# Kernel tuning notes

Measured on AMD Instinct MI355X. Metric: run time of the kernel, lower is better.

## Reference

```python
import jax, jax.numpy as jnp
import numpy as np

FEATURE_DIM = 256
NUM_COEDGES = 200000


def setup_inputs() -> dict:
    key = jax.random.key(0)
    ks = jax.random.split(key, 13)
    d = FEATURE_DIM
    n = NUM_COEDGES
    scale = 1.0 / np.sqrt(d)
    inp = {
        "features": jax.random.normal(ks[0], (n, d), dtype=jnp.float32),
        "next_indices": jax.random.randint(ks[1], (n,), 0, n),
        "prev_indices": jax.random.randint(ks[2], (n,), 0, n),
        "mate_indices": jax.random.randint(ks[3], (n,), 0, n),
        # Linear params (torch Linear: y = x @ W.T + b); store as [d, d] for x @ W
        "W_self": jax.random.uniform(ks[4], (d, d), jnp.float32, -scale, scale),
        "b_self": jax.random.uniform(ks[5], (d,), jnp.float32, -scale, scale),
        "W_next": jax.random.uniform(ks[6], (d, d), jnp.float32, -scale, scale),
        "b_next": jax.random.uniform(ks[7], (d,), jnp.float32, -scale, scale),
        "W_prev": jax.random.uniform(ks[8], (d, d), jnp.float32, -scale, scale),
        "b_prev": jax.random.uniform(ks[9], (d,), jnp.float32, -scale, scale),
        "W_mate": jax.random.uniform(ks[10], (d, d), jnp.float32, -scale, scale),
        "b_mate": jax.random.uniform(ks[11], (d,), jnp.float32, -scale, scale),
    }
    return inp


def reference(features, next_indices, prev_indices, mate_indices,
              W_self, b_self, W_next, b_next, W_prev, b_prev, W_mate, b_mate):
    h = features  # [n, d]
    h_self = h @ W_self + b_self
    h_next = h[next_indices] @ W_next + b_next
    h_prev = h[prev_indices] @ W_prev + b_prev
    h_mate = h[mate_indices] @ W_mate + b_mate
    return jax.nn.relu(h_self + h_next + h_prev + h_mate)
```

## Files before the change

### kernel.cpp

```cpp
#include <hip/hip_runtime.h>
#include <stdint.h>


#define D 256
#define BM 64

typedef __bf16 bf16x8 __attribute__((ext_vector_type(8)));
typedef float f32x4 __attribute__((ext_vector_type(4)));

static __device__ __forceinline__ uint16_t f32_to_bf16_rne(uint32_t u) {
    return (uint16_t)((u + 0x7FFFu + ((u >> 16) & 1u)) >> 16);
}

__global__ void k_conv(const float* __restrict__ f, uint16_t* __restrict__ o, long total) {
    long i = ((long)blockIdx.x * blockDim.x + threadIdx.x) * 8;
    if (i + 8 > total) return;
    const uint32_t* p = (const uint32_t*)(f + i);
    uint32_t v[8];
    *(uint4*)(v)     = *(const uint4*)(p);
    *(uint4*)(v + 4) = *(const uint4*)(p + 4);
    union { uint16_t u16[8]; uint4 v4; } r;
#pragma unroll
    for (int j = 0; j < 8; j++) r.u16[j] = f32_to_bf16_rne(v[j]);
    *(uint4*)(o + i) = r.v4;
}

__global__ void k_pack(const float* __restrict__ Ws, const float* __restrict__ Wn,
                       const float* __restrict__ Wp, const float* __restrict__ Wm,
                       uint16_t* __restrict__ Bp) {
    int b = blockIdx.x;
    int l = threadIdx.x;
    int ksg = b >> 4, nt = b & 15;
    int ph = ksg >> 3;
    const float* W = (ph == 0) ? Ws : (ph == 1) ? Wn : (ph == 2) ? Wp : Wm;
    int kl = (ksg & 7) * 32 + (l >> 4) * 8;
    int n  = nt * 16 + (l & 15);
    uint16_t* dst = Bp + ((size_t)b * 64 + l) * 8;
#pragma unroll
    for (int j = 0; j < 8; j++) {
        uint32_t u = __builtin_bit_cast(uint32_t, W[(size_t)(kl + j) * D + n]);
        dst[j] = f32_to_bf16_rne(u);
    }
}

__global__ void k_bias(const float* __restrict__ b0, const float* __restrict__ b1,
                       const float* __restrict__ b2, const float* __restrict__ b3,
                       float* __restrict__ btot) {
    int t = threadIdx.x;
    if (t < D) btot[t] = b0[t] + b1[t] + b2[t] + b3[t];
}

typedef __attribute__((address_space(1))) uint32_t gu32;
typedef __attribute__((address_space(3))) uint32_t lu32;

__global__ __launch_bounds__(256) void k_gemm(
    const uint16_t* __restrict__ fb,
    const int* __restrict__ ni, const int* __restrict__ pi, const int* __restrict__ mi,
    const uint16_t* __restrict__ Bp, const float* __restrict__ btot,
    float* __restrict__ out, int nrows)
{
    __shared__ uint16_t As[BM * D];
    const int t  = threadIdx.x;
    const int w  = t >> 6;
    const int l  = t & 63;
    const int ml = l & 15;
    const int q  = l >> 4;
    const int m0 = blockIdx.x * BM;

    f32x4 acc[4][4] = {};

    const int rpar = w * 16 + (l >> 5);
    const int cs   = l & 31;

    for (int p = 0; p < 4; p++) {
        const int* idx = (p == 0) ? (const int*)0 : (p == 1) ? ni : (p == 2) ? pi : mi;
        __syncthreads();
#pragma unroll
        for (int e = 0; e < 8; e++) {
            int r    = rpar + e * 2;
            int rowg = m0 + r;
            if (rowg >= nrows) rowg = nrows - 1;
            int gr = idx ? idx[rowg] : rowg;
            int cc = cs ^ (r & 7);
            const uint16_t* g = fb + (size_t)gr * D + cc * 8;
            uint16_t* s = &As[(w * 16 + e * 2) * D];
            __builtin_amdgcn_global_load_lds((gu32*)g, (lu32*)s, 16, 0, 0);
        }
        __syncthreads();

        const uint16_t* bbase = Bp + (((size_t)p * 128 + w * 4) * 64 + l) * 8;
#pragma unroll 2
        for (int ks = 0; ks < 8; ks++) {
            bf16x8 bfr[4];
#pragma unroll
            for (int j = 0; j < 4; j++)
                bfr[j] = *(const bf16x8*)(bbase + ((size_t)ks * 16 + j) * 64 * 8);
            bf16x8 afr[4];
#pragma unroll
            for (int mt = 0; mt < 4; mt++) {
                int r  = mt * 16 + ml;
                int ch = (ks * 4 + q) ^ (r & 7);
                afr[mt] = *(const bf16x8*)&As[r * D + ch * 8];
            }
#pragma unroll
            for (int mt = 0; mt < 4; mt++)
#pragma unroll
                for (int j = 0; j < 4; j++)
                    acc[mt][j] = __builtin_amdgcn_mfma_f32_16x16x32_bf16(
                        afr[mt], bfr[j], acc[mt][j], 0, 0, 0);
        }
    }

#pragma unroll
    for (int j = 0; j < 4; j++) {
        int n = (w * 4 + j) * 16 + ml;
        float bv = btot[n];
#pragma unroll
        for (int mt = 0; mt < 4; mt++) {
#pragma unroll
            for (int rg = 0; rg < 4; rg++) {
                int row = m0 + mt * 16 + q * 4 + rg;
                if (row < nrows) {
                    float v = acc[mt][j][rg] + bv;
                    out[(size_t)row * D + n] = v > 0.f ? v : 0.f;
                }
            }
        }
    }
}

__global__ void k_naive(const float* __restrict__ f,
                        const int* __restrict__ ni, const int* __restrict__ pi,
                        const int* __restrict__ mi,
                        const float* __restrict__ Ws, const float* __restrict__ bs,
                        const float* __restrict__ Wn, const float* __restrict__ bn,
                        const float* __restrict__ Wp, const float* __restrict__ bp,
                        const float* __restrict__ Wm, const float* __restrict__ bm,
                        float* __restrict__ out) {
    int row = blockIdx.x, n = threadIdx.x;
    const float* f0 = f + (size_t)row * D;
    const float* f1 = f + (size_t)ni[row] * D;
    const float* f2 = f + (size_t)pi[row] * D;
    const float* f3 = f + (size_t)mi[row] * D;
    float s = bs[n] + bn[n] + bp[n] + bm[n];
    for (int k = 0; k < D; k++)
        s += f0[k] * Ws[k * D + n] + f1[k] * Wn[k * D + n] +
             f2[k] * Wp[k * D + n] + f3[k] * Wm[k * D + n];
    out[(size_t)row * D + n] = s > 0.f ? s : 0.f;
}

extern "C" void kernel_launch(void* const* d_in, const int* in_sizes, int n_in,
                              void* d_out, int out_size, void* d_ws, size_t ws_size,
                              hipStream_t stream) {
    const float* feat = (const float*)d_in[0];
    const int*   ni   = (const int*)d_in[1];
    const int*   pi   = (const int*)d_in[2];
    const int*   mi   = (const int*)d_in[3];
    const float* Ws   = (const float*)d_in[4];
    const float* bs   = (const float*)d_in[5];
    const float* Wn   = (const float*)d_in[6];
    const float* bn   = (const float*)d_in[7];
    const float* Wp   = (const float*)d_in[8];
    const float* bp   = (const float*)d_in[9];
    const float* Wm   = (const float*)d_in[10];
    const float* bm   = (const float*)d_in[11];
    float* out = (float*)d_out;

    int nrows = in_sizes[1];
    size_t feat_elems = (size_t)nrows * D;
    size_t fb_bytes   = feat_elems * 2;
    size_t bp_off     = fb_bytes;
    size_t bias_off   = bp_off + (size_t)1024 * D * 2;
    size_t need       = bias_off + (size_t)D * 4;

    if (ws_size < need) {
        k_naive<<<nrows, D, 0, stream>>>(feat, ni, pi, mi, Ws, bs, Wn, bn, Wp, bp, Wm, bm, out);
        return;
    }

    uint16_t* fbuf = (uint16_t*)d_ws;
    uint16_t* Bpk  = (uint16_t*)((char*)d_ws + bp_off);
    float*    btot = (float*)((char*)d_ws + bias_off);

    long total = (long)feat_elems;
    int cblocks = (int)((total / 8 + 255) / 256);
    k_conv<<<cblocks, 256, 0, stream>>>(feat, fbuf, total);
    k_pack<<<512, 64, 0, stream>>>(Ws, Wn, Wp, Wm, Bpk);
    k_bias<<<1, 256, 0, stream>>>(bs, bn, bp, bm, btot);
    k_gemm<<<(nrows + BM - 1) / BM, 256, 0, stream>>>(fbuf, ni, pi, mi, Bpk, btot, out, nrows);
}
```

Baseline: 568.6 us.

## Double-buffer gathered A tiles in LDS and fuse prep kernels into one

```diff
diff --git a/kernel.cpp b/kernel.cpp
--- a/kernel.cpp
+++ b/kernel.cpp
@@ -12,54 +12,76 @@
     return (uint16_t)((u + 0x7FFFu + ((u >> 16) & 1u)) >> 16);
 }
 
-__global__ void k_conv(const float* __restrict__ f, uint16_t* __restrict__ o, long total) {
-    long i = ((long)blockIdx.x * blockDim.x + threadIdx.x) * 8;
-    if (i + 8 > total) return;
-    const uint32_t* p = (const uint32_t*)(f + i);
-    uint32_t v[8];
-    *(uint4*)(v)     = *(const uint4*)(p);
-    *(uint4*)(v + 4) = *(const uint4*)(p + 4);
-    union { uint16_t u16[8]; uint4 v4; } r;
-#pragma unroll
-    for (int j = 0; j < 8; j++) r.u16[j] = f32_to_bf16_rne(v[j]);
-    *(uint4*)(o + i) = r.v4;
-}
-
-__global__ void k_pack(const float* __restrict__ Ws, const float* __restrict__ Wn,
+__global__ void k_prep(const float* __restrict__ f, uint16_t* __restrict__ o, long total,
+                       const float* __restrict__ Ws, const float* __restrict__ Wn,
                        const float* __restrict__ Wp, const float* __restrict__ Wm,
-                       uint16_t* __restrict__ Bp) {
-    int b = blockIdx.x;
-    int l = threadIdx.x;
-    int ksg = b >> 4, nt = b & 15;
-    int ph = ksg >> 3;
-    const float* W = (ph == 0) ? Ws : (ph == 1) ? Wn : (ph == 2) ? Wp : Wm;
-    int kl = (ksg & 7) * 32 + (l >> 4) * 8;
-    int n  = nt * 16 + (l & 15);
-    uint16_t* dst = Bp + ((size_t)b * 64 + l) * 8;
-#pragma unroll
-    for (int j = 0; j < 8; j++) {
-        uint32_t u = __builtin_bit_cast(uint32_t, W[(size_t)(kl + j) * D + n]);
-        dst[j] = f32_to_bf16_rne(u);
-    }
-}
-
-__global__ void k_bias(const float* __restrict__ b0, const float* __restrict__ b1,
+                       uint16_t* __restrict__ Bp,
+                       const float* __restrict__ b0, const float* __restrict__ b1,
                        const float* __restrict__ b2, const float* __restrict__ b3,
                        float* __restrict__ btot) {
-    int t = threadIdx.x;
-    if (t < D) btot[t] = b0[t] + b1[t] + b2[t] + b3[t];
+    long i = ((long)blockIdx.x * blockDim.x + threadIdx.x) * 8;
+    if (i + 8 <= total) {
+        const uint32_t* p = (const uint32_t*)(f + i);
+        uint32_t v[8];
+        *(uint4*)(v)     = *(const uint4*)(p);
+        *(uint4*)(v + 4) = *(const uint4*)(p + 4);
+        union { uint16_t u16[8]; uint4 v4; } r;
+#pragma unroll
+        for (int j = 0; j < 8; j++) r.u16[j] = f32_to_bf16_rne(v[j]);
+        *(uint4*)(o + i) = r.v4;
+    }
+    if (blockIdx.x < 128) {
+        int b = blockIdx.x * 4 + (threadIdx.x >> 6);
+        int l = threadIdx.x & 63;
+        int ksg = b >> 4, nt = b & 15;
+        int ph = ksg >> 3;
+        const float* W = (ph == 0) ? Ws : (ph == 1) ? Wn : (ph == 2) ? Wp : Wm;
+        int kl = (ksg & 7) * 32 + (l >> 4) * 8;
+        int n  = nt * 16 + (l & 15);
+        uint16_t* dst = Bp + ((size_t)b * 64 + l) * 8;
+#pragma unroll
+        for (int j = 0; j < 8; j++) {
+            uint32_t u = __builtin_bit_cast(uint32_t, W[(size_t)(kl + j) * D + n]);
+            dst[j] = f32_to_bf16_rne(u);
+        }
+    } else if (blockIdx.x == 128) {
+        int t = threadIdx.x;
+        if (t < D) btot[t] = b0[t] + b1[t] + b2[t] + b3[t];
+    }
 }
 
 typedef __attribute__((address_space(1))) uint32_t gu32;
 typedef __attribute__((address_space(3))) uint32_t lu32;
 
-__global__ __launch_bounds__(256) void k_gemm(
+static __device__ __forceinline__ void stage(const uint16_t* __restrict__ fb,
+                                             const int* __restrict__ idx,
+                                             int m0, int w, int l,
+                                             uint16_t* buf, int nrows) {
+#pragma unroll
+    for (int e = 0; e < 8; e++) {
+        int rr = w * 16 + e * 2;
+        int i0 = m0 + rr;
+        if (i0 + 1 >= nrows) i0 = nrows - 2;
+        int g0 = idx ? idx[i0]     : i0;
+        int g1 = idx ? idx[i0 + 1] : i0 + 1;
+        int hi = (l >> 5) & 1;
+        int gr = hi ? g1 : g0;
+        int r  = rr + hi;
+        int cc = (l & 31) ^ (r & 7);
+        const uint16_t* g = fb + (size_t)gr * D + cc * 8;
+        uint16_t* s = buf + rr * D;
+        __builtin_amdgcn_global_load_lds((gu32*)g, (lu32*)s, 16, 0, 0);
+    }
+}
+
+__global__ __launch_bounds__(256, 2) void k_gemm(
     const uint16_t* __restrict__ fb,
     const int* __restrict__ ni, const int* __restrict__ pi, const int* __restrict__ mi,
     const uint16_t* __restrict__ Bp, const float* __restrict__ btot,
     float* __restrict__ out, int nrows)
 {
-    __shared__ uint16_t As[BM * D];
+    __shared__ __align__(16) uint16_t As0[BM * D];
+    __shared__ __align__(16) uint16_t As1[BM * D];
     const int t  = threadIdx.x;
     const int w  = t >> 6;
     const int l  = t & 63;
@@ -68,48 +90,52 @@
     const int m0 = blockIdx.x * BM;
 
     f32x4 acc[4][4] = {};
-
-    const int rpar = w * 16 + (l >> 5);
-    const int cs   = l & 31;
-
-    for (int p = 0; p < 4; p++) {
-        const int* idx = (p == 0) ? (const int*)0 : (p == 1) ? ni : (p == 2) ? pi : mi;
-        __syncthreads();
-#pragma unroll
-        for (int e = 0; e < 8; e++) {
-            int r    = rpar + e * 2;
-            int rowg = m0 + r;
-            if (rowg >= nrows) rowg = nrows - 1;
-            int gr = idx ? idx[rowg] : rowg;
-            int cc = cs ^ (r & 7);
-            const uint16_t* g = fb + (size_t)gr * D + cc * 8;
-            uint16_t* s = &As[(w * 16 + e * 2) * D];
-            __builtin_amdgcn_global_load_lds((gu32*)g, (lu32*)s, 16, 0, 0);
-        }
-        __syncthreads();
-
-        const uint16_t* bbase = Bp + (((size_t)p * 128 + w * 4) * 64 + l) * 8;
-#pragma unroll 2
-        for (int ks = 0; ks < 8; ks++) {
-            bf16x8 bfr[4];
-#pragma unroll
-            for (int j = 0; j < 4; j++)
-                bfr[j] = *(const bf16x8*)(bbase + ((size_t)ks * 16 + j) * 64 * 8);
-            bf16x8 afr[4];
-#pragma unroll
-            for (int mt = 0; mt < 4; mt++) {
-                int r  = mt * 16 + ml;
-                int ch = (ks * 4 + q) ^ (r & 7);
-                afr[mt] = *(const bf16x8*)&As[r * D + ch * 8];
-            }
-#pragma unroll
-            for (int mt = 0; mt < 4; mt++)
-#pragma unroll
-                for (int j = 0; j < 4; j++)
-                    acc[mt][j] = __builtin_amdgcn_mfma_f32_16x16x32_bf16(
-                        afr[mt], bfr[j], acc[mt][j], 0, 0, 0);
-        }
-    }
+    bf16x8 Breg[32];
+
+    const uint16_t* bwave = Bp + (((size_t)w * 4) * 64 + l) * 8;
+
+#define LOADB(p)                                                        \
+    {                                                                   \
+        const uint16_t* bb = bwave + (size_t)(p) * 128 * 64 * 8;        \
+        _Pragma("unroll")                                               \
+        for (int ks = 0; ks < 8; ks++)                                  \
+            _Pragma("unroll")                                           \
+            for (int j = 0; j < 4; j++)                                 \
+                Breg[ks * 4 + j] =                                      \
+                    *(const bf16x8*)(bb + ((size_t)(ks * 16 + j)) * 64 * 8); \
+    }
+
+#define COMPUTE(buf)                                                    \
+    {                                                                   \
+        _Pragma("unroll")                                               \
+        for (int ks = 0; ks < 8; ks++) {                                \
+            bf16x8 afr[4];                                              \
+            _Pragma("unroll")                                           \
+            for (int mt = 0; mt < 4; mt++) {                            \
+                int r  = mt * 16 + ml;                                  \
+                int ch = (ks * 4 + q) ^ (r & 7);                        \
+                afr[mt] = *(const bf16x8*)&(buf)[r * D + ch * 8];       \
+            }                                                           \
+            _Pragma("unroll")                                           \
+            for (int mt = 0; mt < 4; mt++)                              \
+                _Pragma("unroll")                                       \
+                for (int j = 0; j < 4; j++)                             \
+                    acc[mt][j] = __builtin_amdgcn_mfma_f32_16x16x32_bf16( \
+                        afr[mt], Breg[ks * 4 + j], acc[mt][j], 0, 0, 0);\
+        }                                                               \
+    }
+
+    stage(fb, (const int*)0, m0, w, l, As0, nrows);
+    stage(fb, ni,            m0, w, l, As1, nrows);
+    __syncthreads();
+
+    LOADB(0); COMPUTE(As0);
+    __syncthreads();
+    LOADB(1); stage(fb, pi, m0, w, l, As0, nrows); COMPUTE(As1);
+    __syncthreads();
+    LOADB(2); stage(fb, mi, m0, w, l, As1, nrows); COMPUTE(As0);
+    __syncthreads();
+    LOADB(3); COMPUTE(As1);
 
 #pragma unroll
     for (int j = 0; j < 4; j++) {
@@ -127,6 +153,8 @@
             }
         }
     }
+#undef LOADB
+#undef COMPUTE
 }
 
 __global__ void k_naive(const float* __restrict__ f,
@@ -184,8 +212,8 @@
 
     long total = (long)feat_elems;
     int cblocks = (int)((total / 8 + 255) / 256);
-    k_conv<<<cblocks, 256, 0, stream>>>(feat, fbuf, total);
-    k_pack<<<512, 64, 0, stream>>>(Ws, Wn, Wp, Wm, Bpk);
-    k_bias<<<1, 256, 0, stream>>>(bs, bn, bp, bm, btot);
+    if (cblocks < 129) cblocks = 129;
+    k_prep<<<cblocks, 256, 0, stream>>>(feat, fbuf, total, Ws, Wn, Wp, Wm, Bpk,
+                                        bs, bn, bp, bm, btot);
     k_gemm<<<(nrows + BM - 1) / BM, 256, 0, stream>>>(fbuf, ni, pi, mi, Bpk, btot, out, nrows);
 }
```

Result: no change. 578.2 us (+1.7%).
